# Kernel tuning notes

Hardware: AMD Instinct MI355X
Metric: run time of the kernel (lower is better)

Reference implementation:

```python
import jax, jax.numpy as jnp
import numpy as np

B, C, N, K = 8, 128, 16384, 8


def setup_inputs() -> dict:
    key = jax.random.key(0)
    ks = jax.random.split(key, 20)
    s = 1.0 / np.sqrt(C)
    def mat(k_, shape, scale):
        return jax.random.normal(k_, shape, jnp.float32) * scale
    return {
        "x": jax.random.normal(ks[0], (B, C, N, 1), jnp.float32),
        "logits": jax.random.normal(ks[1], (B, N), jnp.float32),
        "Wq1": mat(ks[2], (C, C), s), "Wk1": mat(ks[3], (C, C), s), "Wv1": mat(ks[4], (C, C), s),
        "Wq2": mat(ks[5], (C, C), s), "Wk2": mat(ks[6], (C, C), s), "Wv2": mat(ks[7], (C, C), s),
        "Wq3": mat(ks[8], (C, C), s), "Wk3": mat(ks[9], (C, C), s), "Wv3": mat(ks[10], (C, C), s),
        "ln_w": jnp.ones((C,), jnp.float32), "ln_b": jnp.zeros((C,), jnp.float32),
        "conv0_w": mat(ks[11], (C, C), s), "conv0_b": jnp.zeros((C,), jnp.float32),
        "bn_w": jnp.ones((C,), jnp.float32), "bn_b": jnp.zeros((C,), jnp.float32),
        "fc1_w": mat(ks[12], (C // 2, C), s), "fc1_b": jnp.zeros((C // 2,), jnp.float32),
        "fc2_w": mat(ks[13], (C, C // 2), 1.0 / np.sqrt(C // 2)), "fc2_b": jnp.zeros((C,), jnp.float32),
        "k": K,
    }


def _transformer(f, Wq, Wk, Wv):
    # f: [B, C, n] ; 1x1 convs over channel dim
    q = jnp.einsum('oc,bcn->bon', Wq, f)
    kk = jnp.einsum('oc,bcn->bon', Wk, f)
    v = jnp.einsum('oc,bcn->bon', Wv, f)
    temp = jnp.sqrt(jnp.asarray(f.shape[1], f.dtype))
    attn = jax.nn.softmax(jnp.einsum('bcn,bdn->bcd', q / temp, kk), axis=-1)  # [B,C,C]
    return jnp.einsum('bcd,bdn->bcn', attn, v)


def _layernorm_over_c(f, w, b):
    # f: [B, C, n]; original transposes to [B, n, C], LayerNorm(C, eps=1e-6), back
    ft = jnp.swapaxes(f, 1, 2)
    mu = ft.mean(-1, keepdims=True)
    var = ft.var(-1, keepdims=True)
    ft = (ft - mu) * jax.lax.rsqrt(var + 1e-6) * w + b
    return jnp.swapaxes(ft, 1, 2)


def reference(x, logits, Wq1, Wk1, Wv1, Wq2, Wk2, Wv2, Wq3, Wk3, Wv3,
              ln_w, ln_b, conv0_w, conv0_b, bn_w, bn_b, fc1_w, fc1_b, fc2_w, fc2_b, k):
    # --- tanh-threshold binning into k buckets ---
    w = jnp.tanh(logits)                       # [B, N]
    flag = 2.0 / k
    lows = -1.0 + flag * jnp.arange(k, dtype=x.dtype)   # [k]
    highs = lows + flag
    wb = w[None, :, :]                         # [1, B, N]
    # transforto0_1: in (l, r], and original zeros stay zero
    masks = ((wb > lows[:, None, None]) & (wb <= highs[:, None, None]) & (wb != 0)).astype(x.dtype)  # [k,B,N]
    nums = masks.sum(-1)                       # [k, B]
    nums = jnp.where(nums == 0, 1.0, nums)

    x2 = x[..., 0]                             # [B, C, N]
    # masked segment pooling (mean per bin), no channel-broadcast repeat
    pooled = jnp.einsum('bcn,kbn->bck', x2, masks)        # [B, C, k]
    feature = pooled / nums.T[:, None, :]                 # [B, C, k]

    # --- three tiny attention blocks with residual + LN ---
    for Wq, Wk, Wv in ((Wq1, Wk1, Wv1), (Wq2, Wk2, Wv2), (Wq3, Wk3, Wv3)):
        out = _transformer(feature, Wq, Wk, Wv) + feature
        feature = _layernorm_over_c(out, ln_w, ln_b)

    # --- scatter-add reconstruction: sum_i mask_i*x + mask_i*level_i ---
    total = masks.sum(0)                                  # [B, N]
    recon = x2 * total[:, None, :] + jnp.einsum('bck,kbn->bcn', feature, masks)
    result = recon[..., None]                             # [B, C, N, 1]

    # --- SE block ---
    mu_i = result.mean(axis=(2, 3), keepdims=True)
    var_i = result.var(axis=(2, 3), keepdims=True)
    h = (result - mu_i) * jax.lax.rsqrt(var_i + 1e-5)     # InstanceNorm2d
    mu_b = h.mean(axis=(0, 2, 3), keepdims=True)
    var_b = h.var(axis=(0, 2, 3), keepdims=True)
    h = (h - mu_b) * jax.lax.rsqrt(var_b + 1e-5)          # BatchNorm2d (batch stats)
    h = h * bn_w[None, :, None, None] + bn_b[None, :, None, None]
    h = jax.nn.gelu(h, approximate=False)
    conv = jnp.einsum('oc,bcnp->bonp', conv0_w, h) + conv0_b[None, :, None, None]
    sq = conv.reshape(conv.shape[0], conv.shape[1], -1).mean(-1)   # [B, C]
    f1 = jax.nn.gelu(sq @ fc1_w.T + fc1_b, approximate=False)
    f2 = jax.nn.sigmoid(f1 @ fc2_w.T + fc2_b)
    return conv * f2[:, :, None, None]
```

## Files before the change

kernel.cpp:

```cpp
#include <hip/hip_runtime.h>
#include <math.h>

#define Bdim 8
#define Cdim 128
#define Ndim 16384
#define Kdim 8

typedef __attribute__((ext_vector_type(8))) short short8;
typedef __attribute__((ext_vector_type(4))) float f32x4;

__device__ __forceinline__ unsigned rne16(float x) {
  unsigned u = __float_as_uint(x);
  return (u + 0x7FFFu + ((u >> 16) & 1u)) >> 16;
}

__global__ void __launch_bounds__(256) k_bin(const float* __restrict__ logits,
                                             signed char* __restrict__ kbin,
                                             int* __restrict__ cnt) {
  __shared__ int h[Kdim];
  int tid = threadIdx.x;
  if (tid < Kdim) h[tid] = 0;
  __syncthreads();
  int idx = blockIdx.x * 256 + tid;
  int b = idx >> 14;
  float w = tanhf(logits[idx]);
  int kb = -1;
#pragma unroll
  for (int j = 0; j < Kdim; ++j) {
    float lo = -1.0f + 0.25f * (float)j;
    float hi = lo + 0.25f;
    if (w > lo && w <= hi && w != 0.0f) kb = j;
  }
  kbin[idx] = (signed char)kb;
  if (kb >= 0) atomicAdd(&h[kb], 1);
  __syncthreads();
  if (tid < Kdim) atomicAdd(&cnt[b * Kdim + tid], h[tid]);
}

__global__ void __launch_bounds__(256) k_pool(const float* __restrict__ x,
                                              const signed char* __restrict__ kbin,
                                              float* __restrict__ pooled,
                                              float* __restrict__ sxx) {
  int bc = blockIdx.x;
  int b = bc >> 7;
  const float4* xr = (const float4*)(x + (size_t)bc * Ndim);
  const char4* kr = (const char4*)(kbin + b * Ndim);
  float acc[Kdim];
#pragma unroll
  for (int j = 0; j < Kdim; ++j) acc[j] = 0.f;
  float s2 = 0.f;
  int tid = threadIdx.x;
  for (int n4 = tid; n4 < Ndim / 4; n4 += 256) {
    float4 v = xr[n4];
    char4 kb = kr[n4];
    float ve[4] = {v.x, v.y, v.z, v.w};
    signed char ke[4] = {kb.x, kb.y, kb.z, kb.w};
#pragma unroll
    for (int e = 0; e < 4; ++e) {
      float xv = ve[e];
      int kv = ke[e];
      if (kv >= 0) s2 += xv * xv;
#pragma unroll
      for (int j = 0; j < Kdim; ++j) acc[j] += (kv == j) ? xv : 0.f;
    }
  }
#pragma unroll
  for (int off = 32; off > 0; off >>= 1) {
#pragma unroll
    for (int j = 0; j < Kdim; ++j) acc[j] += __shfl_down(acc[j], off);
    s2 += __shfl_down(s2, off);
  }
  __shared__ float red[4][Kdim + 1];
  int wv = tid >> 6, ln = tid & 63;
  if (ln == 0) {
#pragma unroll
    for (int j = 0; j < Kdim; ++j) red[wv][j] = acc[j];
    red[wv][Kdim] = s2;
  }
  __syncthreads();
  if (tid < Kdim) pooled[bc * Kdim + tid] = red[0][tid] + red[1][tid] + red[2][tid] + red[3][tid];
  if (tid == Kdim) sxx[bc] = red[0][Kdim] + red[1][Kdim] + red[2][Kdim] + red[3][Kdim];
}

__global__ void __launch_bounds__(256) k_wprep(
    const float* __restrict__ p0, const float* __restrict__ p1, const float* __restrict__ p2,
    const float* __restrict__ p3, const float* __restrict__ p4, const float* __restrict__ p5,
    const float* __restrict__ p6, const float* __restrict__ p7, const float* __restrict__ p8,
    unsigned short* __restrict__ Wbf) {
  int m = blockIdx.x >> 6;
  int i = (blockIdx.x & 63) * 256 + threadIdx.x;
  const float* mp = m == 0 ? p0 : m == 1 ? p1 : m == 2 ? p2 : m == 3 ? p3 : m == 4 ? p4
                  : m == 5 ? p5 : m == 6 ? p6 : m == 7 ? p7 : p8;
  Wbf[m * 16384 + i] = (unsigned short)rne16(mp[i]);
}

__global__ void __launch_bounds__(256) k_warm(const unsigned short* __restrict__ Wbf,
                                              float* __restrict__ dummy) {
  int g = blockIdx.x >> 3;
  int t = threadIdx.x;
  int idx = g * 256 + t;
  uint4 v = ((const uint4*)Wbf)[idx];
  float s = (float)(v.x ^ v.y ^ v.z ^ v.w);
#pragma unroll
  for (int off = 32; off > 0; off >>= 1) s += __shfl_down(s, off);
  if ((t & 63) == 0) dummy[blockIdx.x * 4 + (t >> 6)] = s;
}

__global__ void __launch_bounds__(1024) k_xform(
    const float* __restrict__ pooled, const int* __restrict__ cnt,
    const float* __restrict__ sxx, const unsigned short* __restrict__ Wbf,
    const float* __restrict__ ln_w, const float* __restrict__ ln_b,
    float* __restrict__ feat, float* __restrict__ mu_i, float* __restrict__ rs_i,
    float* __restrict__ ratio) {
  __shared__ float f_l[Kdim][132], q_l[Kdim][132], kk_l[Kdim][132], v_l[Kdim][132];
  __shared__ unsigned short fTh[16][132], fTl[16][132];
  __shared__ float part[Kdim][Kdim][Cdim];
  __shared__ float pm[Kdim][Cdim], ps[Kdim][Cdim];
  __shared__ float lnw_l[Cdim], lnb_l[Cdim];
  __shared__ float cnt_raw[Kdim], cnt_div[Kdim];
  __shared__ float redA[Kdim][2], redB[Kdim][2];
  int b = blockIdx.x, tid = threadIdx.x;
  int c_ = tid & 127, h_ = tid >> 7;
  int o8 = tid >> 3, j8 = tid & 7;
  int wid = tid >> 6, lane = tid & 63;
  int l15 = lane & 15, lg = lane >> 4;
  const float inv_temp = 0.08838834764831845f;

  if (tid < Kdim) {
    int cc = cnt[b * Kdim + tid];
    cnt_raw[tid] = (float)cc;
    cnt_div[tid] = (float)(cc == 0 ? 1 : cc);
  }
  if (tid >= 128 && tid < 256) lnw_l[tid - 128] = ln_w[tid - 128];
  if (tid >= 256 && tid < 384) lnb_l[tid - 256] = ln_b[tid - 256];
  __syncthreads();
  {
    float fv = pooled[(b * Cdim + o8) * Kdim + j8] / cnt_div[j8];
    f_l[j8][o8] = fv;
    unsigned hi = rne16(fv);
    fTh[j8][o8] = (unsigned short)hi;
    fTl[j8][o8] = (unsigned short)rne16(fv - __uint_as_float(hi << 16));
  }
  float t_carry = 0.f;
  float sv[16];
  float mloc = 0.f;
  for (int layer = 0; layer < 3; ++layer) {
    if (layer > 0) {
      float S1 = redA[h_][0] + redA[h_][1];
      float S2 = redB[h_][0] + redB[h_][1];
      float mu = S1 * (1.f / Cdim);
      float var = S2 * (1.f / Cdim) - mu * mu;
      float rs = rsqrtf(var + 1e-6f);
      float fv = (t_carry - mu) * rs * lnw_l[c_] + lnb_l[c_];
      f_l[h_][c_] = fv;
      unsigned hi = rne16(fv);
      fTh[h_][c_] = (unsigned short)hi;
      fTl[h_][c_] = (unsigned short)rne16(fv - __uint_as_float(hi << 16));
    }
    __syncthreads();
    for (int job = wid; job < 24; job += 16) {
      int m = job >> 3, ot = job & 7;
      const unsigned short* A = Wbf + (size_t)(layer * 3 + m) * 16384 + (ot * 16 + l15) * 128;
      f32x4 acc = (f32x4){0.f, 0.f, 0.f, 0.f};
#pragma unroll
      for (int ks = 0; ks < 4; ++ks) {
        int kbase = ks * 32 + lg * 8;
        short8 a = *(const short8*)(A + kbase);
        short8 bh = *(const short8*)&fTh[l15][kbase];
        short8 bl = *(const short8*)&fTl[l15][kbase];
        acc = __builtin_amdgcn_mfma_f32_16x16x32_bf16(a, bh, acc, 0, 0, 0);
        acc = __builtin_amdgcn_mfma_f32_16x16x32_bf16(a, bl, acc, 0, 0, 0);
      }
      if (l15 < 8) {
#pragma unroll
        for (int r = 0; r < 4; ++r) {
          int o = ot * 16 + lg * 4 + r;
          float v = acc[r];
          if (m == 0) q_l[l15][o] = v * inv_temp;
          else if (m == 1) kk_l[l15][o] = v;
          else v_l[l15][o] = v;
        }
      }
    }
    __syncthreads();
    {
      int d0 = h_ * 16;
      float qv[8];
#pragma unroll
      for (int j = 0; j < 8; ++j) qv[j] = q_l[j][c_];
#pragma unroll
      for (int dd = 0; dd < 16; ++dd) sv[dd] = 0.f;
#pragma unroll
      for (int j = 0; j < 8; ++j) {
#pragma unroll
        for (int d4 = 0; d4 < 4; ++d4) {
          float4 k4 = *(const float4*)&kk_l[j][d0 + d4 * 4];
          sv[d4 * 4 + 0] = fmaf(qv[j], k4.x, sv[d4 * 4 + 0]);
          sv[d4 * 4 + 1] = fmaf(qv[j], k4.y, sv[d4 * 4 + 1]);
          sv[d4 * 4 + 2] = fmaf(qv[j], k4.z, sv[d4 * 4 + 2]);
          sv[d4 * 4 + 3] = fmaf(qv[j], k4.w, sv[d4 * 4 + 3]);
        }
      }
      mloc = sv[0];
#pragma unroll
      for (int dd = 1; dd < 16; ++dd) mloc = fmaxf(mloc, sv[dd]);
      float sl = 0.f;
#pragma unroll
      for (int dd = 0; dd < 16; ++dd) {
        sv[dd] = expf(sv[dd] - mloc);
        sl += sv[dd];
      }
      pm[h_][c_] = mloc;
      ps[h_][c_] = sl;
    }
    __syncthreads();
    {
      float M = pm[0][c_];
#pragma unroll
      for (int hh = 1; hh < 8; ++hh) M = fmaxf(M, pm[hh][c_]);
      float S = 0.f;
#pragma unroll
      for (int hh = 0; hh < 8; ++hh) S += ps[hh][c_] * expf(pm[hh][c_] - M);
      float fac = expf(mloc - M) / S;
#pragma unroll
      for (int dd = 0; dd < 16; ++dd) sv[dd] *= fac;
      int d0 = h_ * 16;
#pragma unroll
      for (int j = 0; j < 8; ++j) {
        float po = 0.f;
#pragma unroll
        for (int d4 = 0; d4 < 4; ++d4) {
          float4 v4 = *(const float4*)&v_l[j][d0 + d4 * 4];
          po = fmaf(sv[d4 * 4 + 0], v4.x, po);
          po = fmaf(sv[d4 * 4 + 1], v4.y, po);
          po = fmaf(sv[d4 * 4 + 2], v4.z, po);
          po = fmaf(sv[d4 * 4 + 3], v4.w, po);
        }
        part[h_][j][c_] = po;
      }
    }
    __syncthreads();
    {
      float t = f_l[h_][c_];
#pragma unroll
      for (int hh = 0; hh < 8; ++hh) t += part[hh][h_][c_];
      t_carry = t;
      float s1 = t, s2 = t * t;
#pragma unroll
      for (int off = 32; off > 0; off >>= 1) {
        s1 += __shfl_xor(s1, off);
        s2 += __shfl_xor(s2, off);
      }
      int wv = (tid >> 6) & 1;
      if ((tid & 63) == 0) { redA[h_][wv] = s1; redB[h_][wv] = s2; }
    }
    __syncthreads();
  }
  {
    float S1 = redA[h_][0] + redA[h_][1];
    float S2 = redB[h_][0] + redB[h_][1];
    float mu = S1 * (1.f / Cdim);
    float var = S2 * (1.f / Cdim) - mu * mu;
    float rs = rsqrtf(var + 1e-6f);
    f_l[h_][c_] = (t_carry - mu) * rs * lnw_l[c_] + lnb_l[c_];
  }
  __syncthreads();
  if (tid < Cdim) {
    int c = tid;
    float S1 = 0.f, S2c = 0.f;
#pragma unroll
    for (int j = 0; j < Kdim; ++j) {
      float pl = pooled[(b * Cdim + c) * Kdim + j];
      float fe = f_l[j][c];
      feat[(b * Cdim + c) * Kdim + j] = fe;
      S1 += pl + cnt_raw[j] * fe;
      S2c += 2.f * pl * fe + cnt_raw[j] * fe * fe;
    }
    float S2 = sxx[b * Cdim + c] + S2c;
    float mu = S1 * (1.f / Ndim);
    float var = S2 * (1.f / Ndim) - mu * mu;
    float rs = rsqrtf(var + 1e-5f);
    mu_i[b * Cdim + c] = mu;
    rs_i[b * Cdim + c] = rs;
    ratio[b * Cdim + c] = var * rs * rs;
  }
}

__global__ void k_alpha(const float* __restrict__ mu_i, const float* __restrict__ rs_i,
                        const float* __restrict__ ratio, const float* __restrict__ bn_w,
                        const float* __restrict__ bn_b, float* __restrict__ alpha,
                        float* __restrict__ beta) {
  int c = threadIdx.x;
  float vb = 0.f;
  for (int b = 0; b < Bdim; ++b) vb += ratio[b * Cdim + c];
  vb *= (1.f / Bdim);
  float rsb = rsqrtf(vb + 1e-5f);
  float w = bn_w[c], bb = bn_b[c];
  for (int b = 0; b < Bdim; ++b) {
    float a = rs_i[b * Cdim + c] * rsb * w;
    alpha[b * Cdim + c] = a;
    beta[b * Cdim + c] = bb - mu_i[b * Cdim + c] * a;
  }
}

__global__ void k_wsplit(const float* __restrict__ W, unsigned short* __restrict__ Wh,
                         unsigned short* __restrict__ Wl, unsigned short* __restrict__ Whs,
                         unsigned short* __restrict__ Wls) {
  int idx = blockIdx.x * 256 + threadIdx.x;
  int o = idx >> 7, c = idx & 127;
  float v = W[idx];
  unsigned u = __float_as_uint(v);
  unsigned rh = (u + 0x7FFFu + ((u >> 16) & 1u)) & 0xFFFF0000u;
  float vh = __uint_as_float(rh);
  float r = v - vh;
  unsigned u2 = __float_as_uint(r);
  unsigned rl = (u2 + 0x7FFFu + ((u2 >> 16) & 1u)) >> 16;
  unsigned short hs = (unsigned short)(rh >> 16);
  unsigned short ls = (unsigned short)rl;
  Wh[idx] = hs;
  Wl[idx] = ls;
  int pos = o * 128 + (((c >> 3) ^ (o & 7)) << 3) + (c & 7);
  Whs[pos] = hs;
  Wls[pos] = ls;
}

__global__ void __launch_bounds__(256) k_gpack(
    const float* __restrict__ x, const signed char* __restrict__ kbin,
    const float* __restrict__ feat,
    const float* __restrict__ mu_i, const float* __restrict__ rs_i,
    const float* __restrict__ ratio, const float* __restrict__ bn_w,
    const float* __restrict__ bn_b, unsigned short* __restrict__ gpack,
    float* __restrict__ gsum) {
  __shared__ unsigned short xg[Cdim][132];
  __shared__ float feat_l[Cdim][Kdim];
  __shared__ float al_l[Cdim], be_l[Cdim];
  __shared__ signed char kb_l[128];
  int tile = blockIdx.x;
  int b = tile >> 7, nb = tile & 127;
  int n0 = nb * 128;
  int t = threadIdx.x;
  for (int idx = t; idx < Cdim * Kdim; idx += 256)
    ((float*)feat_l)[idx] = feat[b * Cdim * Kdim + idx];
  if (t < 128) {
    int c = t;
    float vb = 0.f;
#pragma unroll
    for (int bb = 0; bb < Bdim; ++bb) vb += ratio[bb * Cdim + c];
    vb *= (1.f / Bdim);
    float rsb = rsqrtf(vb + 1e-5f);
    float a = rs_i[b * Cdim + c] * rsb * bn_w[c];
    al_l[c] = a;
    be_l[c] = bn_b[c] - mu_i[b * Cdim + c] * a;
    kb_l[c] = kbin[b * Ndim + n0 + c];
  }
  __syncthreads();
#pragma unroll 4
  for (int it = 0; it < 16; ++it) {
    int idx = it * 256 + t;
    int q = idx & 31, c = idx >> 5;
    float4 xv = *(const float4*)(x + ((size_t)(b * Cdim + c)) * Ndim + n0 + q * 4);
    float a = al_l[c], be = be_l[c];
    float xe[4] = {xv.x, xv.y, xv.z, xv.w};
    unsigned short rr[4];
#pragma unroll
    for (int e = 0; e < 4; ++e) {
      int kb = kb_l[q * 4 + e];
      float rec = (kb >= 0) ? (xe[e] + feat_l[c][kb]) : 0.0f;
      float h = fmaf(a, rec, be);
      float g = 0.5f * h * (1.0f + erff(h * 0.7071067811865475244f));
      rr[e] = (unsigned short)rne16(g);
    }
    *(ushort4*)&xg[c][q * 4] = make_ushort4(rr[0], rr[1], rr[2], rr[3]);
  }
  __syncthreads();
  {
    int c = t >> 1, half = t & 1;
    float s = 0.f;
#pragma unroll 8
    for (int i = 0; i < 64; ++i) {
      unsigned us = xg[c][half * 64 + i];
      s += __uint_as_float(us << 16);
    }
    s += __shfl_xor(s, 1);
    if (half == 0) atomicAdd(&gsum[b * Cdim + c], s);
  }
  unsigned short* tb = gpack + (size_t)tile * 16384;
#pragma unroll 2
  for (int it = 0; it < 8; ++it) {
    int idx = it * 256 + t;
    int cg = idx & 15, n = idx >> 4;
    unsigned u32s[4];
#pragma unroll
    for (int p = 0; p < 4; ++p) {
      unsigned lo = xg[cg * 8 + 2 * p][n];
      unsigned hi = xg[cg * 8 + 2 * p + 1][n];
      u32s[p] = lo | (hi << 16);
    }
    int g = cg ^ (n & 7);
    *(uint4*)(tb + n * 128 + g * 8) = make_uint4(u32s[0], u32s[1], u32s[2], u32s[3]);
  }
}

__global__ void __launch_bounds__(256) k_gmean(
    const float* __restrict__ x, const signed char* __restrict__ kbin,
    const float* __restrict__ feat, const float* __restrict__ alpha,
    const float* __restrict__ beta, float* __restrict__ gmean) {
  int bc = blockIdx.x;
  int b = bc >> 7;
  __shared__ float fl[Kdim];
  int tid = threadIdx.x;
  if (tid < Kdim) fl[tid] = feat[bc * Kdim + tid];
  __syncthreads();
  float a = alpha[bc], be = beta[bc];
  const float4* xr = (const float4*)(x + (size_t)bc * Ndim);
  const char4* kr = (const char4*)(kbin + b * Ndim);
  float s = 0.f;
  for (int n4 = tid; n4 < Ndim / 4; n4 += 256) {
    float4 v = xr[n4];
    char4 kb = kr[n4];
    float ve[4] = {v.x, v.y, v.z, v.w};
    signed char ke[4] = {kb.x, kb.y, kb.z, kb.w};
#pragma unroll
    for (int e = 0; e < 4; ++e) {
      int kv = ke[e];
      float rec = 0.f;
#pragma unroll
      for (int j = 0; j < Kdim; ++j) rec += (kv == j) ? (ve[e] + fl[j]) : 0.f;
      float h = fmaf(a, rec, be);
      s += 0.5f * h * (1.0f + erff(h * 0.7071067811865475244f));
    }
  }
#pragma unroll
  for (int off = 32; off > 0; off >>= 1) s += __shfl_down(s, off);
  __shared__ float red[4];
  int wv = tid >> 6;
  if ((tid & 63) == 0) red[wv] = s;
  __syncthreads();
  if (tid == 0) gmean[bc] = (red[0] + red[1] + red[2] + red[3]) * (1.0f / Ndim);
}

__global__ void __launch_bounds__(128) k_mlp(const float* __restrict__ gmean,
                                             const float* __restrict__ W,
                                             const float* __restrict__ conv_b,
                                             const float* __restrict__ fc1w,
                                             const float* __restrict__ fc1b,
                                             const float* __restrict__ fc2w,
                                             const float* __restrict__ fc2b,
                                             float inv,
                                             float* __restrict__ f2g) {
  __shared__ float gm[Cdim];
  __shared__ float sq[Cdim];
  __shared__ float f1[64];
  int b = blockIdx.x, tid = threadIdx.x;
  gm[tid] = gmean[b * Cdim + tid] * inv;
  __syncthreads();
  float a = conv_b[tid];
  const float* wr = W + tid * Cdim;
  for (int c = 0; c < Cdim; ++c) a = fmaf(wr[c], gm[c], a);
  sq[tid] = a;
  __syncthreads();
  if (tid < 64) {
    float a1 = fc1b[tid];
    for (int c = 0; c < Cdim; ++c) a1 = fmaf(fc1w[tid * Cdim + c], sq[c], a1);
    f1[tid] = 0.5f * a1 * (1.0f + erff(a1 * 0.7071067811865475244f));
  }
  __syncthreads();
  float a2 = fc2b[tid];
  for (int i = 0; i < 64; ++i) a2 = fmaf(fc2w[tid * 64 + i], f1[i], a2);
  f2g[b * Cdim + tid] = 1.0f / (1.0f + expf(-a2));
}

__global__ void __launch_bounds__(1024) k_conv_g(
    const unsigned short* __restrict__ gpack,
    const unsigned short* __restrict__ Whs, const unsigned short* __restrict__ Wls,
    const float* __restrict__ bias, const float* __restrict__ f2g,
    float* __restrict__ out) {
  __shared__ unsigned short Whl[16384];
  __shared__ unsigned short Wll[16384];
  __shared__ unsigned short Bb[2][16384];
  __shared__ float bi_l[Cdim], f2_l[Cdim];
  int t = threadIdx.x;
  int blk = blockIdx.x;
  int b = blk >> 5;
  int tile0 = blk * 4;
  if (t < 128) {
    bi_l[t] = bias[t];
    f2_l[t] = f2g[b * Cdim + t];
  }
  {
    const uint4* gw = (const uint4*)Whs;
    const uint4* gl = (const uint4*)Wls;
    const uint4* gb = (const uint4*)(gpack + (size_t)tile0 * 16384);
    uint4* lw = (uint4*)Whl;
    uint4* ll = (uint4*)Wll;
    uint4* lb = (uint4*)Bb[0];
    lw[t] = gw[t]; lw[t + 1024] = gw[t + 1024];
    ll[t] = gl[t]; ll[t + 1024] = gl[t + 1024];
    lb[t] = gb[t]; lb[t + 1024] = gb[t + 1024];
  }
  __syncthreads();
  int w = t >> 6, lane = t & 63;
  int wo = (w & 1) * 64, wn = (w >> 1) * 16;
  int l15 = lane & 15, lg = lane >> 4;
  int nrow = wn + l15;
  int brow = nrow * 128;
  int bswz = nrow & 7;
  int cur = 0;
  for (int tt = 0; tt < 4; ++tt) {
    uint4 rb0, rb1;
    if (tt < 3) {
      const uint4* gb = (const uint4*)(gpack + (size_t)(tile0 + tt + 1) * 16384);
      rb0 = gb[t];
      rb1 = gb[t + 1024];
    }
    f32x4 acc[4];
#pragma unroll
    for (int of = 0; of < 4; ++of) acc[of] = (f32x4){0.f, 0.f, 0.f, 0.f};
#pragma unroll
    for (int kb = 0; kb < 4; ++kb) {
      int g = kb * 4 + lg;
      short8 bb = *(const short8*)&Bb[cur][brow + ((g ^ bswz) << 3)];
#pragma unroll
      for (int of = 0; of < 4; ++of) {
        int o = wo + of * 16 + l15;
        int apos = o * 128 + ((g ^ (o & 7)) << 3);
        short8 ah = *(const short8*)&Whl[apos];
        short8 al_ = *(const short8*)&Wll[apos];
        acc[of] = __builtin_amdgcn_mfma_f32_16x16x32_bf16(ah, bb, acc[of], 0, 0, 0);
        acc[of] = __builtin_amdgcn_mfma_f32_16x16x32_bf16(al_, bb, acc[of], 0, 0, 0);
      }
    }
    __syncthreads();
    if (tt < 3) {
      uint4* lb = (uint4*)Bb[cur ^ 1];
      lb[t] = rb0;
      lb[t + 1024] = rb1;
    }
    __syncthreads();
    int n0 = ((tile0 + tt) & 127) * 128;
#pragma unroll
    for (int of = 0; of < 4; ++of) {
#pragma unroll
      for (int r = 0; r < 4; ++r) {
        int o = wo + of * 16 + lg * 4 + r;
        out[((size_t)(b * Cdim + o)) * Ndim + n0 + wn + l15] =
            (acc[of][r] + bi_l[o]) * f2_l[o];
      }
    }
    cur ^= 1;
  }
}

__global__ void __launch_bounds__(512, 4) k_conv_x(
    const float* __restrict__ x, const signed char* __restrict__ kbin,
    const float* __restrict__ feat, const float* __restrict__ alpha,
    const float* __restrict__ beta,
    const unsigned short* __restrict__ Wh, const unsigned short* __restrict__ Wl,
    const float* __restrict__ bias, const float* __restrict__ f2g,
    float* __restrict__ out) {
  __shared__ unsigned g_hl[Cdim][132];
  __shared__ float feat_l[Cdim][Kdim];
  __shared__ float al_l[Cdim], be_l[Cdim], f2_l[Cdim], bi_l[Cdim];
  __shared__ signed char kb_l[128];
  int bx = blockIdx.x;
  int b = bx >> 7, nb = bx & 127;
  int n0 = nb * 128;
  int tid = threadIdx.x;
  for (int idx = tid; idx < Cdim * Kdim; idx += 512)
    ((float*)feat_l)[idx] = feat[b * Cdim * Kdim + idx];
  if (tid < Cdim) {
    al_l[tid] = alpha[b * Cdim + tid];
    be_l[tid] = beta[b * Cdim + tid];
    f2_l[tid] = f2g[b * Cdim + tid];
    bi_l[tid] = bias[tid];
  }
  if (tid >= 256 && tid < 384) kb_l[tid - 256] = kbin[b * Ndim + n0 + (tid - 256)];
  __syncthreads();
  for (int idx = tid; idx < Cdim * 32; idx += 512) {
    int c = idx >> 5, q4 = idx & 31;
    float4 xv = *(const float4*)(x + ((size_t)(b * Cdim + c)) * Ndim + n0 + q4 * 4);
    float a = al_l[c], be = be_l[c];
    float xe[4] = {xv.x, xv.y, xv.z, xv.w};
    unsigned r[4];
#pragma unroll
    for (int e = 0; e < 4; ++e) {
      int kb = kb_l[q4 * 4 + e];
      float rec = (kb >= 0) ? (xe[e] + feat_l[c][kb]) : 0.0f;
      float h = fmaf(a, rec, be);
      float g = 0.5f * h * (1.0f + erff(h * 0.7071067811865475244f));
      unsigned u = __float_as_uint(g);
      unsigned rh = (u + 0x7FFFu + ((u >> 16) & 1u)) & 0xFFFF0000u;
      float rr = g - __uint_as_float(rh);
      unsigned u2 = __float_as_uint(rr);
      unsigned rl = (u2 + 0x7FFFu + ((u2 >> 16) & 1u)) >> 16;
      r[e] = rh | rl;
    }
    int p4 = (q4 * 4) ^ (((c >> 3) & 1) << 4);
    *(uint4*)&g_hl[c][p4] = make_uint4(r[0], r[1], r[2], r[3]);
  }
  __syncthreads();
  int wid = tid >> 6, lane = tid & 63;
  int wo = (wid & 1) * 64;
  int wn = (wid >> 1) * 32;
  int l15 = lane & 15, lg = lane >> 4;
  f32x4 acc[4][2];
#pragma unroll
  for (int of = 0; of < 4; ++of)
#pragma unroll
    for (int nf = 0; nf < 2; ++nf) acc[of][nf] = (f32x4){0.f, 0.f, 0.f, 0.f};
#pragma unroll 2
  for (int kb = 0; kb < 4; ++kb) {
    int kbase = kb * 32 + lg * 8;
    short8 ah[4], alo[4];
#pragma unroll
    for (int of = 0; of < 4; ++of) {
      int o = wo + of * 16 + l15;
      ah[of] = *(const short8*)(Wh + o * Cdim + kbase);
      alo[of] = *(const short8*)(Wl + o * Cdim + kbase);
    }
#pragma unroll
    for (int nf = 0; nf < 2; ++nf) {
      int n = wn + nf * 16 + l15;
      int par = lg & 1;
      short8 bh, bl;
#pragma unroll
      for (int j = 0; j < 8; ++j) {
        unsigned u = g_hl[kbase + j][n ^ (par << 4)];
        bh[j] = (short)(u >> 16);
        bl[j] = (short)(u & 0xFFFFu);
      }
#pragma unroll
      for (int of = 0; of < 4; ++of) {
        acc[of][nf] = __builtin_amdgcn_mfma_f32_16x16x32_bf16(ah[of], bh, acc[of][nf], 0, 0, 0);
        acc[of][nf] = __builtin_amdgcn_mfma_f32_16x16x32_bf16(ah[of], bl, acc[of][nf], 0, 0, 0);
        acc[of][nf] = __builtin_amdgcn_mfma_f32_16x16x32_bf16(alo[of], bh, acc[of][nf], 0, 0, 0);
      }
    }
  }
#pragma unroll
  for (int of = 0; of < 4; ++of) {
#pragma unroll
    for (int nf = 0; nf < 2; ++nf) {
#pragma unroll
      for (int r = 0; r < 4; ++r) {
        int o = wo + of * 16 + lg * 4 + r;
        int n = wn + nf * 16 + l15;
        out[((size_t)(b * Cdim + o)) * Ndim + n0 + n] = (acc[of][nf][r] + bi_l[o]) * f2_l[o];
      }
    }
  }
}

extern "C" void kernel_launch(void* const* d_in, const int* in_sizes, int n_in,
                              void* d_out, int out_size, void* d_ws, size_t ws_size,
                              hipStream_t stream) {
  const float* x = (const float*)d_in[0];
  const float* logits = (const float*)d_in[1];
  const float* Wq1 = (const float*)d_in[2];
  const float* Wk1 = (const float*)d_in[3];
  const float* Wv1 = (const float*)d_in[4];
  const float* Wq2 = (const float*)d_in[5];
  const float* Wk2 = (const float*)d_in[6];
  const float* Wv2 = (const float*)d_in[7];
  const float* Wq3 = (const float*)d_in[8];
  const float* Wk3 = (const float*)d_in[9];
  const float* Wv3 = (const float*)d_in[10];
  const float* ln_w = (const float*)d_in[11];
  const float* ln_b = (const float*)d_in[12];
  const float* conv0_w = (const float*)d_in[13];
  const float* conv0_b = (const float*)d_in[14];
  const float* bn_w = (const float*)d_in[15];
  const float* bn_b = (const float*)d_in[16];
  const float* fc1_w = (const float*)d_in[17];
  const float* fc1_b = (const float*)d_in[18];
  const float* fc2_w = (const float*)d_in[19];
  const float* fc2_b = (const float*)d_in[20];
  float* out = (float*)d_out;

  char* p = (char*)d_ws;
  auto alloc = [&](size_t bytes) {
    char* r = p;
    p += (bytes + 255) & ~(size_t)255;
    return r;
  };
  signed char* kbin = (signed char*)alloc(Bdim * Ndim);
  int* cnt = (int*)alloc(Bdim * Kdim * 4);
  float* pooled = (float*)alloc(Bdim * Cdim * Kdim * 4);
  float* sxx = (float*)alloc(Bdim * Cdim * 4);
  float* feat = (float*)alloc(Bdim * Cdim * Kdim * 4);
  float* mu_i = (float*)alloc(Bdim * Cdim * 4);
  float* rs_i = (float*)alloc(Bdim * Cdim * 4);
  float* ratio = (float*)alloc(Bdim * Cdim * 4);
  float* alpha = (float*)alloc(Bdim * Cdim * 4);
  float* beta = (float*)alloc(Bdim * Cdim * 4);
  unsigned short* Wh = (unsigned short*)alloc(Cdim * Cdim * 2);
  unsigned short* Wlo = (unsigned short*)alloc(Cdim * Cdim * 2);
  unsigned short* Whs = (unsigned short*)alloc(Cdim * Cdim * 2);
  unsigned short* Wls = (unsigned short*)alloc(Cdim * Cdim * 2);
  unsigned short* Wbf = (unsigned short*)alloc(9 * Cdim * Cdim * 2);
  float* f2g = (float*)alloc(Bdim * Cdim * 4);
  float* gmean = (float*)alloc(Bdim * Cdim * 4);
  float* warmdummy = (float*)alloc(576 * 4 * 4);
  unsigned short* gpack = (unsigned short*)alloc((size_t)Bdim * Cdim * Ndim * 2);
  bool fast = ((size_t)(p - (char*)d_ws) <= ws_size);

  hipMemsetAsync(cnt, 0, Bdim * Kdim * sizeof(int), stream);
  k_bin<<<Bdim * Ndim / 256, 256, 0, stream>>>(logits, kbin, cnt);
  k_wsplit<<<Cdim * Cdim / 256, 256, 0, stream>>>(conv0_w, Wh, Wlo, Whs, Wls);
  k_wprep<<<9 * 64, 256, 0, stream>>>(Wq1, Wk1, Wv1, Wq2, Wk2, Wv2, Wq3, Wk3, Wv3, Wbf);
  k_pool<<<Bdim * Cdim, 256, 0, stream>>>(x, kbin, pooled, sxx);
  k_warm<<<576, 256, 0, stream>>>(Wbf, warmdummy);
  k_xform<<<Bdim, 1024, 0, stream>>>(pooled, cnt, sxx, Wbf, ln_w, ln_b,
                                     feat, mu_i, rs_i, ratio);
  if (fast) {
    hipMemsetAsync(gmean, 0, Bdim * Cdim * sizeof(float), stream);
    k_gpack<<<Bdim * 128, 256, 0, stream>>>(x, kbin, feat, mu_i, rs_i, ratio, bn_w, bn_b,
                                            gpack, gmean);
    k_mlp<<<Bdim, 128, 0, stream>>>(gmean, conv0_w, conv0_b, fc1_w, fc1_b, fc2_w, fc2_b,
                                    1.0f / Ndim, f2g);
    k_conv_g<<<256, 1024, 0, stream>>>(gpack, Whs, Wls, conv0_b, f2g, out);
  } else {
    k_alpha<<<1, 128, 0, stream>>>(mu_i, rs_i, ratio, bn_w, bn_b, alpha, beta);
    k_gmean<<<Bdim * Cdim, 256, 0, stream>>>(x, kbin, feat, alpha, beta, gmean);
    k_mlp<<<Bdim, 128, 0, stream>>>(gmean, conv0_w, conv0_b, fc1_w, fc1_b, fc2_w, fc2_b,
                                    1.0f, f2g);
    k_conv_x<<<Bdim * (Ndim / 128), 512, 0, stream>>>(x, kbin, feat, alpha, beta, Wh, Wlo,
                                                      conv0_b, f2g, out);
  }
}
```

Measured before the change: 126.7 us.

## Merge weight-prep kernels and memsets, use polynomial GELU, fuse channel sums

Combines the conv weight split, the QKV bf16 conversion and both memsets into a single prep kernel, cutting two kernel launches and two memset nodes. In k_gpack, exact erf GELU is replaced by an Abramowitz-Stegun polynomial with __expf, which is cheaper on the ALU but approximate (error around 1e-7 before bf16 rounding). The per-channel sum is now accumulated inside the conversion loop through wave shuffles and atomics, removing a shared-memory rescan pass and a barrier. The cost is more atomics: one per 32 lanes per iteration instead of one per channel.

```diff
diff --git a/kernel.cpp b/kernel.cpp
--- a/kernel.cpp
+++ b/kernel.cpp
@@ -12,6 +12,53 @@
 __device__ __forceinline__ unsigned rne16(float x) {
   unsigned u = __float_as_uint(x);
   return (u + 0x7FFFu + ((u >> 16) & 1u)) >> 16;
+}
+
+__device__ __forceinline__ float fast_gelu(float h) {
+  float z = fabsf(h) * 0.70710678118654752440f;
+  float t = 1.0f / fmaf(0.3275911f, z, 1.0f);
+  float p = t * fmaf(t, fmaf(t, fmaf(t, fmaf(t, 1.061405429f, -1.453152027f),
+                                     1.421413741f), -0.284496736f), 0.254829592f);
+  float er = fmaf(-p, __expf(-z * z), 1.0f);
+  float phi = 0.5f + copysignf(0.5f * er, h);
+  return h * phi;
+}
+
+__global__ void __launch_bounds__(256) k_prep(
+    const float* __restrict__ W, unsigned short* __restrict__ Wh,
+    unsigned short* __restrict__ Wl, unsigned short* __restrict__ Whs,
+    unsigned short* __restrict__ Wls,
+    const float* __restrict__ p0, const float* __restrict__ p1, const float* __restrict__ p2,
+    const float* __restrict__ p3, const float* __restrict__ p4, const float* __restrict__ p5,
+    const float* __restrict__ p6, const float* __restrict__ p7, const float* __restrict__ p8,
+    unsigned short* __restrict__ Wbf, int* __restrict__ cnt, float* __restrict__ gmean) {
+  int blk = blockIdx.x, t = threadIdx.x;
+  if (blk < 64) {
+    int idx = blk * 256 + t;
+    int o = idx >> 7, c = idx & 127;
+    float v = W[idx];
+    unsigned u = __float_as_uint(v);
+    unsigned rh = (u + 0x7FFFu + ((u >> 16) & 1u)) & 0xFFFF0000u;
+    float vh = __uint_as_float(rh);
+    float r = v - vh;
+    unsigned u2 = __float_as_uint(r);
+    unsigned rl = (u2 + 0x7FFFu + ((u2 >> 16) & 1u)) >> 16;
+    unsigned short hs = (unsigned short)(rh >> 16);
+    unsigned short ls = (unsigned short)rl;
+    Wh[idx] = hs;
+    Wl[idx] = ls;
+    int pos = o * 128 + (((c >> 3) ^ (o & 7)) << 3) + (c & 7);
+    Whs[pos] = hs;
+    Wls[pos] = ls;
+    if (blk == 0 && t < Bdim * Kdim) cnt[t] = 0;
+    if (blk < 4) gmean[blk * 256 + t] = 0.f;
+  } else {
+    int m = (blk - 64) >> 6;
+    int i = ((blk - 64) & 63) * 256 + t;
+    const float* mp = m == 0 ? p0 : m == 1 ? p1 : m == 2 ? p2 : m == 3 ? p3 : m == 4 ? p4
+                    : m == 5 ? p5 : m == 6 ? p6 : m == 7 ? p7 : p8;
+    Wbf[m * 16384 + i] = (unsigned short)rne16(mp[i]);
+  }
 }
 
 __global__ void __launch_bounds__(256) k_bin(const float* __restrict__ logits,
@@ -80,18 +127,6 @@
   __syncthreads();
   if (tid < Kdim) pooled[bc * Kdim + tid] = red[0][tid] + red[1][tid] + red[2][tid] + red[3][tid];
   if (tid == Kdim) sxx[bc] = red[0][Kdim] + red[1][Kdim] + red[2][Kdim] + red[3][Kdim];
-}
-
-__global__ void __launch_bounds__(256) k_wprep(
-    const float* __restrict__ p0, const float* __restrict__ p1, const float* __restrict__ p2,
-    const float* __restrict__ p3, const float* __restrict__ p4, const float* __restrict__ p5,
-    const float* __restrict__ p6, const float* __restrict__ p7, const float* __restrict__ p8,
-    unsigned short* __restrict__ Wbf) {
-  int m = blockIdx.x >> 6;
-  int i = (blockIdx.x & 63) * 256 + threadIdx.x;
-  const float* mp = m == 0 ? p0 : m == 1 ? p1 : m == 2 ? p2 : m == 3 ? p3 : m == 4 ? p4
-                  : m == 5 ? p5 : m == 6 ? p6 : m == 7 ? p7 : p8;
-  Wbf[m * 16384 + i] = (unsigned short)rne16(mp[i]);
 }
 
 __global__ void __launch_bounds__(256) k_warm(const unsigned short* __restrict__ Wbf,
@@ -301,27 +336,6 @@
     alpha[b * Cdim + c] = a;
     beta[b * Cdim + c] = bb - mu_i[b * Cdim + c] * a;
   }
-}
-
-__global__ void k_wsplit(const float* __restrict__ W, unsigned short* __restrict__ Wh,
-                         unsigned short* __restrict__ Wl, unsigned short* __restrict__ Whs,
-                         unsigned short* __restrict__ Wls) {
-  int idx = blockIdx.x * 256 + threadIdx.x;
-  int o = idx >> 7, c = idx & 127;
-  float v = W[idx];
-  unsigned u = __float_as_uint(v);
-  unsigned rh = (u + 0x7FFFu + ((u >> 16) & 1u)) & 0xFFFF0000u;
-  float vh = __uint_as_float(rh);
-  float r = v - vh;
-  unsigned u2 = __float_as_uint(r);
-  unsigned rl = (u2 + 0x7FFFu + ((u2 >> 16) & 1u)) >> 16;
-  unsigned short hs = (unsigned short)(rh >> 16);
-  unsigned short ls = (unsigned short)rl;
-  Wh[idx] = hs;
-  Wl[idx] = ls;
-  int pos = o * 128 + (((c >> 3) ^ (o & 7)) << 3) + (c & 7);
-  Whs[pos] = hs;
-  Wls[pos] = ls;
 }
 
 __global__ void __launch_bounds__(256) k_gpack(
@@ -362,28 +376,26 @@
     float a = al_l[c], be = be_l[c];
     float xe[4] = {xv.x, xv.y, xv.z, xv.w};
     unsigned short rr[4];
+    float s_it = 0.f;
 #pragma unroll
     for (int e = 0; e < 4; ++e) {
       int kb = kb_l[q * 4 + e];
       float rec = (kb >= 0) ? (xe[e] + feat_l[c][kb]) : 0.0f;
       float h = fmaf(a, rec, be);
-      float g = 0.5f * h * (1.0f + erff(h * 0.7071067811865475244f));
-      rr[e] = (unsigned short)rne16(g);
+      float g = fast_gelu(h);
+      unsigned gb = rne16(g);
+      rr[e] = (unsigned short)gb;
+      s_it += __uint_as_float(gb << 16);
     }
     *(ushort4*)&xg[c][q * 4] = make_ushort4(rr[0], rr[1], rr[2], rr[3]);
-  }
-  __syncthreads();
-  {
-    int c = t >> 1, half = t & 1;
-    float s = 0.f;
-#pragma unroll 8
-    for (int i = 0; i < 64; ++i) {
-      unsigned us = xg[c][half * 64 + i];
-      s += __uint_as_float(us << 16);
-    }
-    s += __shfl_xor(s, 1);
-    if (half == 0) atomicAdd(&gsum[b * Cdim + c], s);
-  }
+    s_it += __shfl_xor(s_it, 1);
+    s_it += __shfl_xor(s_it, 2);
+    s_it += __shfl_xor(s_it, 4);
+    s_it += __shfl_xor(s_it, 8);
+    s_it += __shfl_xor(s_it, 16);
+    if ((t & 31) == 0) atomicAdd(&gsum[b * Cdim + c], s_it);
+  }
+  __syncthreads();
   unsigned short* tb = gpack + (size_t)tile * 16384;
 #pragma unroll 2
   for (int it = 0; it < 8; ++it) {
@@ -704,16 +716,15 @@
   unsigned short* gpack = (unsigned short*)alloc((size_t)Bdim * Cdim * Ndim * 2);
   bool fast = ((size_t)(p - (char*)d_ws) <= ws_size);
 
-  hipMemsetAsync(cnt, 0, Bdim * Kdim * sizeof(int), stream);
+  k_prep<<<640, 256, 0, stream>>>(conv0_w, Wh, Wlo, Whs, Wls,
+                                  Wq1, Wk1, Wv1, Wq2, Wk2, Wv2, Wq3, Wk3, Wv3,
+                                  Wbf, cnt, gmean);
   k_bin<<<Bdim * Ndim / 256, 256, 0, stream>>>(logits, kbin, cnt);
-  k_wsplit<<<Cdim * Cdim / 256, 256, 0, stream>>>(conv0_w, Wh, Wlo, Whs, Wls);
-  k_wprep<<<9 * 64, 256, 0, stream>>>(Wq1, Wk1, Wv1, Wq2, Wk2, Wv2, Wq3, Wk3, Wv3, Wbf);
   k_pool<<<Bdim * Cdim, 256, 0, stream>>>(x, kbin, pooled, sxx);
   k_warm<<<576, 256, 0, stream>>>(Wbf, warmdummy);
   k_xform<<<Bdim, 1024, 0, stream>>>(pooled, cnt, sxx, Wbf, ln_w, ln_b,
                                      feat, mu_i, rs_i, ratio);
   if (fast) {
-    hipMemsetAsync(gmean, 0, Bdim * Cdim * sizeof(float), stream);
     k_gpack<<<Bdim * 128, 256, 0, stream>>>(x, kbin, feat, mu_i, rs_i, ratio, bn_w, bn_b,
                                             gpack, gmean);
     k_mlp<<<Bdim, 128, 0, stream>>>(gmean, conv0_w, conv0_b, fc1_w, fc1_b, fc2_w, fc2_b,
```

Measured after the change: 148.6 us. +17.3%, slower.
